# Kernel optimization log

Hardware: AMD Instinct MI355X
Metric: run time of the kernel (lower is better)

The kernel has to match this reference:

```python
import jax, jax.numpy as jnp
import numpy as np

EPS = 1e-5

def layer_norm(x, w, b):
    mu = x.mean(-1, keepdims=True)
    var = x.var(-1, keepdims=True)
    return (x - mu) / jnp.sqrt(var + EPS) * w + b

def moe_ffn(y, gW, W1, b1, W2, b2, topk):
    # y: [B,N,d]; W1: [E,d,f]; W2: [E,f,d].  Dense-equivalent of the
    # torch gather/compute/scatter-add dispatch: every expert runs on every
    # token, combined with top-k gate weights (zero for unselected experts).
    gate = jax.nn.softmax(y @ gW, axis=-1)                       # [B,N,E]
    w, sel = jax.lax.top_k(gate, topk)                           # [B,N,k]
    onehot = jax.nn.one_hot(sel, gW.shape[-1], dtype=y.dtype)    # [B,N,k,E]
    comb = jnp.einsum('bnk,bnke->bne', w, onehot)                # combine weights
    hmid = jax.nn.gelu(jnp.einsum('bnd,edf->bnef', y, W1) + b1, approximate=False)
    eo = jnp.einsum('bnef,efd->bned', hmid, W2) + b2             # [B,N,E,d]
    out = jnp.einsum('bne,bned->bnd', comb, eo)
    mask = onehot.sum(2)                                         # [B,N,E] 0/1
    cnt = mask.sum((0, 1))                                       # tokens per expert
    emb = jnp.einsum('bne,bnd->ed', mask, y) / jnp.maximum(cnt, 1.0)[:, None]
    return out, gate, emb

def setup_inputs():
    B, S, N = 8, 512, 1024
    d, H, E, f, L, topk = 512, 8, 8, 8, 2, 2   # d_ff == n_heads (repo quirk)
    key = jax.random.key(0)
    ks = iter(jax.random.split(key, 40))
    g = lambda shape, s=0.02: jax.random.normal(next(ks), shape, jnp.float32) * s
    return dict(
        x=jax.random.normal(next(ks), (B, S, N), jnp.float32),
        revin_w=jnp.ones((N,), jnp.float32) + g((N,), 0.01),
        revin_b=g((N,), 0.01),
        emb_W=g((S, d)), emb_b=g((d,)),
        Wq=g((L, d, d)), bq=g((L, d)),
        Wk=g((L, d, d)), bk=g((L, d)),
        Wv=g((L, d, d)), bv=g((L, d)),
        Wo=g((L, d, d)), bo=g((L, d)),
        ln1_w=jnp.ones((L, d), jnp.float32), ln1_b=jnp.zeros((L, d), jnp.float32),
        ln2_w=jnp.ones((L, d), jnp.float32), ln2_b=jnp.zeros((L, d), jnp.float32),
        gate_W=g((L, d, E)),
        eW1=g((L, E, d, f)), eb1=g((L, E, f)),
        eW2=g((L, E, f, d)), eb2=g((L, E, d)),
        enc_norm_w=jnp.ones((d,), jnp.float32), enc_norm_b=jnp.zeros((d,), jnp.float32),
        head_gate_W=g((d, E)),
        head_W=g((E, d, d)), head_b=g((E, d)),
        topk=topk, n_heads=H,
    )

def reference(x, revin_w, revin_b, emb_W, emb_b, Wq, bq, Wk, bk, Wv, bv, Wo, bo,
              ln1_w, ln1_b, ln2_w, ln2_b, gate_W, eW1, eb1, eW2, eb2,
              enc_norm_w, enc_norm_b, head_gate_W, head_W, head_b, topk, n_heads):
    B, S, N = x.shape
    d = emb_W.shape[1]
    H = n_heads
    dh = d // H
    L = Wq.shape[0]
    # RevIN normalize over time per variable (dropout layers are eval/identity)
    xv = jnp.swapaxes(x, 1, 2)                                   # [B,N,S]
    mean = xv.mean(-1, keepdims=True)
    std = jnp.sqrt(xv.var(-1, keepdims=True) + EPS)
    xn = (xv - mean) / std * revin_w[None, :, None] + revin_b[None, :, None]
    # DataEmbedding_inverted: Linear over the time axis -> variable tokens
    h = xn @ emb_W + emb_b                                       # [B,N,d]
    for l in range(L):
        q = (h @ Wq[l] + bq[l]).reshape(B, N, H, dh)
        k = (h @ Wk[l] + bk[l]).reshape(B, N, H, dh)
        v = (h @ Wv[l] + bv[l]).reshape(B, N, H, dh)
        attn = jax.nn.softmax(jnp.einsum('bnhe,bmhe->bhnm', q, k) / jnp.sqrt(jnp.float32(dh)), axis=-1)
        o = jnp.einsum('bhnm,bmhe->bnhe', attn, v).reshape(B, N, d) @ Wo[l] + bo[l]
        h = layer_norm(h + o, ln1_w[l], ln1_b[l])
        ffn, _gate, _emb = moe_ffn(h, gate_W[l], eW1[l], eb1[l], eW2[l], eb2[l], topk)
        h = layer_norm(h + ffn, ln2_w[l], ln2_b[l])
    h = layer_norm(h, enc_norm_w, enc_norm_b)
    # MoE projection head: experts are Linear(d, d)
    gate = jax.nn.softmax(h @ head_gate_W, axis=-1)
    w, sel = jax.lax.top_k(gate, topk)
    onehot = jax.nn.one_hot(sel, head_gate_W.shape[-1], dtype=h.dtype)
    comb = jnp.einsum('bnk,bnke->bne', w, onehot)
    eo = jnp.einsum('bnd,edf->bnef', h, head_W) + head_b         # [B,N,E,d]
    out = jnp.einsum('bne,bned->bnd', comb, eo)                  # [B,N,d]
    # RevIN denorm applied on [B, d_model, N]
    o2 = jnp.swapaxes(out, 1, 2)
    o2 = (o2 - revin_b[None, None, :]) / (revin_w[None, None, :] + 1e-10)
    o2 = o2 * jnp.swapaxes(std, 1, 2) + jnp.swapaxes(mean, 1, 2)
    return jnp.swapaxes(o2, 1, 2)                                # [B, n_vars, d_model]
```

## Files before the change

kernel.cpp:

```cpp
#include <hip/hip_runtime.h>
#include <math.h>

#define BATCH 8
#define SEQ 512
#define NVAR 1024
#define DM 512
#define NH 8
#define DH 64
#define NE 8
#define NF 8
#define NL 2
#define NTOK (BATCH*NVAR)
#define LN_EPS 1e-5f
#define LSC 2048.0f
#define ILSC (1.0f/2048.0f)

typedef __attribute__((ext_vector_type(8))) _Float16 f16x8;
typedef __attribute__((ext_vector_type(4))) float f32x4;
#define MFMA16 __builtin_amdgcn_mfma_f32_16x16x32_f16

__device__ __forceinline__ void fsplit(float v, _Float16& hi, _Float16& lo) {
    hi = (_Float16)v;
    lo = (_Float16)((v - (float)hi) * LSC);
}
__device__ __forceinline__ float frec(_Float16 hi, _Float16 lo) {
    return (float)hi + (float)lo * ILSC;
}

__device__ __forceinline__ void gload_lds16(const _Float16* g, _Float16* l) {
    __builtin_amdgcn_global_load_lds(
        (const __attribute__((address_space(1))) void*)g,
        (__attribute__((address_space(3))) void*)l, 16, 0, 0);
}

#define DPPROR(v, C) __int_as_float(__builtin_amdgcn_update_dpp(0, __float_as_int(v), (C), 0xF, 0xF, true))
__device__ __forceinline__ float rowmax16(float v) {
    v = fmaxf(v, DPPROR(v, 0x121));
    v = fmaxf(v, DPPROR(v, 0x122));
    v = fmaxf(v, DPPROR(v, 0x124));
    v = fmaxf(v, DPPROR(v, 0x128));
    return v;
}
__device__ __forceinline__ float rowsum16(float v) {
    v += DPPROR(v, 0x121);
    v += DPPROR(v, 0x122);
    v += DPPROR(v, 0x124);
    v += DPPROR(v, 0x128);
    return v;
}

__global__ __launch_bounds__(256) void revin_stats_kernel(
        const float* __restrict__ x, float* __restrict__ mean, float* __restrict__ stdd) {
    int blk = blockIdx.x;
    int b = blk >> 4;
    int n0 = (blk & 15) << 6;
    int t = threadIdx.x;
    int ni = t & 63, sg = t >> 6;
    float s = 0.f, ss = 0.f;
    for (int sidx = sg; sidx < SEQ; sidx += 4) {
        float v = x[((size_t)b*SEQ + sidx)*NVAR + n0 + ni];
        s += v; ss += v*v;
    }
    __shared__ float rs[4][64], rq[4][64];
    rs[sg][ni] = s; rq[sg][ni] = ss;
    __syncthreads();
    if (t < 64) {
        float su = rs[0][t] + rs[1][t] + rs[2][t] + rs[3][t];
        float sq = rq[0][t] + rq[1][t] + rq[2][t] + rq[3][t];
        float m  = su / (float)SEQ;
        float var = sq / (float)SEQ - m*m;
        int n = n0 + t;
        mean[b*NVAR + n] = m;
        stdd[b*NVAR + n] = sqrtf(var + LN_EPS);
    }
}

__global__ __launch_bounds__(256) void revin_norm_kernel(
        const float* __restrict__ x, const float* __restrict__ mean, const float* __restrict__ stdd,
        const float* __restrict__ rw, const float* __restrict__ rb,
        _Float16* __restrict__ xnhi, _Float16* __restrict__ xnlo) {
    __shared__ float tile[32][33];
    int n0 = blockIdx.x << 5, s0 = blockIdx.y << 5, b = blockIdx.z;
    int t = threadIdx.x;
    int j = t & 31, i0 = t >> 5;
    for (int ii = i0; ii < 32; ii += 8)
        tile[ii][j] = x[((size_t)b*SEQ + s0 + ii)*NVAR + n0 + j];
    __syncthreads();
    int si = t & 31, j0 = t >> 5;
    for (int nj = j0; nj < 32; nj += 8) {
        int n = n0 + nj;
        float m = mean[b*NVAR + n], sd = stdd[b*NVAR + n];
        float v = (tile[si][nj] - m) / sd * rw[n] + rb[n];
        _Float16 h_, l_; fsplit(v, h_, l_);
        size_t idx = ((size_t)b*NVAR + n)*SEQ + s0 + si;
        xnhi[idx] = h_; xnlo[idx] = l_;
    }
}

struct WSrcs { const float* p[9]; };
__global__ __launch_bounds__(256) void transpose_w_kernel(
        WSrcs srcs, _Float16* __restrict__ whi, _Float16* __restrict__ wlo) {
    const float* W = srcs.p[blockIdx.z];
    _Float16* oh = whi + (size_t)blockIdx.z * DM * DM;
    _Float16* ol = wlo + (size_t)blockIdx.z * DM * DM;
    __shared__ float tile[64][65];
    int k0 = blockIdx.x << 6, n0 = blockIdx.y << 6;
    int t = threadIdx.x;
    for (int idx = t; idx < 4096; idx += 256) {
        int k = idx >> 6, n = idx & 63;
        tile[k][n] = W[(size_t)(k0 + k)*DM + n0 + n];
    }
    __syncthreads();
    for (int idx = t; idx < 4096; idx += 256) {
        int n = idx >> 6, k = idx & 63;
        _Float16 h_, l_; fsplit(tile[k][n], h_, l_);
        size_t o = (size_t)(n0 + n)*DM + k0 + k;
        oh[o] = h_; ol[o] = l_;
    }
}

__global__ __launch_bounds__(256) void gemm_f16x2_kernel(
        const _Float16* __restrict__ Ahg, const _Float16* __restrict__ Alg,
        const _Float16* __restrict__ Whg, const _Float16* __restrict__ Wlg,
        const float* __restrict__ bias, float* __restrict__ C,
        _Float16* __restrict__ Chi, _Float16* __restrict__ Clo,
        int M, int K, int N) {
    __shared__ _Float16 sAh[128][32], sAl[128][32];
    __shared__ _Float16 sBh[64][32],  sBl[64][32];
    int id = blockIdx.x + (blockIdx.y << 3);
    int rm = ((id & 7) << 6) | (id >> 3);
    int bm = (rm >> 3) << 7, bn = (rm & 7) << 6;
    int t = threadIdx.x;
    int w = t >> 6, lane = t & 63, m16 = lane & 15, quad = lane >> 4;
    int wv = __builtin_amdgcn_readfirstlane(w);
    int lrow = lane >> 2, lcol = (lane & 3) << 3;
    f32x4 a1[2][4] = {}, a2[2][4] = {};
    for (int k0 = 0; k0 < K; k0 += 32) {
#pragma unroll
        for (int c = 0; c < 2; ++c) {
            size_t ga = (size_t)(bm + wv*32 + c*16 + lrow)*K + k0 + lcol;
            gload_lds16(&Ahg[ga], &sAh[wv*32 + c*16][0]);
            gload_lds16(&Alg[ga], &sAl[wv*32 + c*16][0]);
        }
        size_t gb = (size_t)(bn + wv*16 + lrow)*K + k0 + lcol;
        gload_lds16(&Whg[gb], &sBh[wv*16][0]);
        gload_lds16(&Wlg[gb], &sBl[wv*16][0]);
        __syncthreads();
        f16x8 bh_[4], bl_[4];
#pragma unroll
        for (int nt = 0; nt < 4; ++nt) {
            bh_[nt] = *(const f16x8*)&sBh[nt*16 + m16][quad*8];
            bl_[nt] = *(const f16x8*)&sBl[nt*16 + m16][quad*8];
        }
#pragma unroll
        for (int h2 = 0; h2 < 2; ++h2) {
            f16x8 ah = *(const f16x8*)&sAh[w*32 + h2*16 + m16][quad*8];
            f16x8 al = *(const f16x8*)&sAl[w*32 + h2*16 + m16][quad*8];
#pragma unroll
            for (int nt = 0; nt < 4; ++nt) {
                a1[h2][nt] = MFMA16(ah, bh_[nt], a1[h2][nt], 0, 0, 0);
                a2[h2][nt] = MFMA16(ah, bl_[nt], a2[h2][nt], 0, 0, 0);
                a2[h2][nt] = MFMA16(al, bh_[nt], a2[h2][nt], 0, 0, 0);
            }
        }
        __syncthreads();
    }
#pragma unroll
    for (int h2 = 0; h2 < 2; ++h2)
#pragma unroll
        for (int nt = 0; nt < 4; ++nt) {
            int col = bn + nt*16 + m16;
            float bv = bias[col];
#pragma unroll
            for (int r = 0; r < 4; ++r) {
                size_t row = bm + w*32 + h2*16 + quad*4 + r;
                float v = a1[h2][nt][r] + a2[h2][nt][r]*ILSC + bv;
                if (C) C[row*N + col] = v;
                if (Chi) {
                    _Float16 h_, l_; fsplit(v, h_, l_);
                    Chi[row*N + col] = h_; Clo[row*N + col] = l_;
                }
            }
        }
}

__global__ __launch_bounds__(256) void gemm_f16x2_vt_kernel(
        const _Float16* __restrict__ Ahg, const _Float16* __restrict__ Alg,
        const _Float16* __restrict__ Whg, const _Float16* __restrict__ Wlg,
        const float* __restrict__ bias,
        _Float16* __restrict__ vthi, _Float16* __restrict__ vtlo) {
    __shared__ _Float16 sAh[128][32], sAl[128][32];
    __shared__ _Float16 sBh[64][32],  sBl[64][32];
    __shared__ float Ct[128][65];
    int id = blockIdx.x + (blockIdx.y << 3);
    int rm = ((id & 7) << 6) | (id >> 3);
    int bm = (rm >> 3) << 7, bn = (rm & 7) << 6;
    int t = threadIdx.x;
    int w = t >> 6, lane = t & 63, m16 = lane & 15, quad = lane >> 4;
    int wv = __builtin_amdgcn_readfirstlane(w);
    int lrow = lane >> 2, lcol = (lane & 3) << 3;
    f32x4 a1[2][4] = {}, a2[2][4] = {};
    for (int k0 = 0; k0 < DM; k0 += 32) {
#pragma unroll
        for (int c = 0; c < 2; ++c) {
            size_t ga = (size_t)(bm + wv*32 + c*16 + lrow)*DM + k0 + lcol;
            gload_lds16(&Ahg[ga], &sAh[wv*32 + c*16][0]);
            gload_lds16(&Alg[ga], &sAl[wv*32 + c*16][0]);
        }
        size_t gb = (size_t)(bn + wv*16 + lrow)*DM + k0 + lcol;
        gload_lds16(&Whg[gb], &sBh[wv*16][0]);
        gload_lds16(&Wlg[gb], &sBl[wv*16][0]);
        __syncthreads();
        f16x8 bh_[4], bl_[4];
#pragma unroll
        for (int nt = 0; nt < 4; ++nt) {
            bh_[nt] = *(const f16x8*)&sBh[nt*16 + m16][quad*8];
            bl_[nt] = *(const f16x8*)&sBl[nt*16 + m16][quad*8];
        }
#pragma unroll
        for (int h2 = 0; h2 < 2; ++h2) {
            f16x8 ah = *(const f16x8*)&sAh[w*32 + h2*16 + m16][quad*8];
            f16x8 al = *(const f16x8*)&sAl[w*32 + h2*16 + m16][quad*8];
#pragma unroll
            for (int nt = 0; nt < 4; ++nt) {
                a1[h2][nt] = MFMA16(ah, bh_[nt], a1[h2][nt], 0, 0, 0);
                a2[h2][nt] = MFMA16(ah, bl_[nt], a2[h2][nt], 0, 0, 0);
                a2[h2][nt] = MFMA16(al, bh_[nt], a2[h2][nt], 0, 0, 0);
            }
        }
        __syncthreads();
    }
#pragma unroll
    for (int h2 = 0; h2 < 2; ++h2)
#pragma unroll
        for (int nt = 0; nt < 4; ++nt) {
            float bv = bias[bn + nt*16 + m16];
#pragma unroll
            for (int r = 0; r < 4; ++r)
                Ct[w*32 + h2*16 + quad*4 + r][nt*16 + m16] = a1[h2][nt][r] + a2[h2][nt][r]*ILSC + bv;
        }
    __syncthreads();
    int b = bm >> 10, tokn0 = bm & 1023, hh = bn >> 6;
    int dh = t >> 2, tg = (t & 3) << 4;
    size_t rowb = ((size_t)(b*8 + hh)*64 + dh)*NVAR + tokn0;
    for (int hb = 0; hb < 2; ++hb) {
        int tl0 = hb*64 + tg;
        unsigned short hbuf[16], lbuf[16];
#pragma unroll
        for (int i = 0; i < 16; ++i) {
            _Float16 h_, l_; fsplit(Ct[tl0 + i][dh], h_, l_);
            hbuf[i] = __builtin_bit_cast(unsigned short, h_);
            lbuf[i] = __builtin_bit_cast(unsigned short, l_);
        }
        uint4 uh0, uh1, ul0, ul1;
        uh0.x = hbuf[0]|(hbuf[1]<<16);  uh0.y = hbuf[2]|(hbuf[3]<<16);
        uh0.z = hbuf[4]|(hbuf[5]<<16);  uh0.w = hbuf[6]|(hbuf[7]<<16);
        uh1.x = hbuf[8]|(hbuf[9]<<16);  uh1.y = hbuf[10]|(hbuf[11]<<16);
        uh1.z = hbuf[12]|(hbuf[13]<<16);uh1.w = hbuf[14]|(hbuf[15]<<16);
        ul0.x = lbuf[0]|(lbuf[1]<<16);  ul0.y = lbuf[2]|(lbuf[3]<<16);
        ul0.z = lbuf[4]|(lbuf[5]<<16);  ul0.w = lbuf[6]|(lbuf[7]<<16);
        ul1.x = lbuf[8]|(lbuf[9]<<16);  ul1.y = lbuf[10]|(lbuf[11]<<16);
        ul1.z = lbuf[12]|(lbuf[13]<<16);ul1.w = lbuf[14]|(lbuf[15]<<16);
        *(uint4*)&vthi[rowb + tl0]     = uh0;
        *(uint4*)&vthi[rowb + tl0 + 8] = uh1;
        *(uint4*)&vtlo[rowb + tl0]     = ul0;
        *(uint4*)&vtlo[rowb + tl0 + 8] = ul1;
    }
}

__global__ __launch_bounds__(256, 4) void attn_f16x2_kernel(
        const _Float16* __restrict__ qh, const _Float16* __restrict__ ql,
        const _Float16* __restrict__ kh, const _Float16* __restrict__ kl,
        const _Float16* __restrict__ vth, const _Float16* __restrict__ vtl,
        _Float16* __restrict__ oh, _Float16* __restrict__ ol) {
    __shared__ _Float16 Kh[64][72], Kl[64][72];
    __shared__ _Float16 Vh[64][72], Vl[64][72];
    int blk = blockIdx.x;
    blk = ((blk & 7) << 7) | (blk >> 3);
    int qt = blk & 15, bh = blk >> 4;
    int b = bh >> 3, hh = bh & 7;
    int q0 = qt << 6;
    int t = threadIdx.x;
    int w = t >> 6, lane = t & 63;
    int m16 = lane & 15, quad = lane >> 4;
    size_t bbase = (size_t)b * NVAR;
    size_t vbase = (size_t)bh * DH * NVAR;

    f16x8 qfh[2], qfl[2];
#pragma unroll
    for (int ks = 0; ks < 2; ++ks) {
        size_t gq = (bbase + q0 + w*16 + m16)*DM + hh*DH + ks*32 + quad*8;
        qfh[ks] = *(const f16x8*)&qh[gq] * (_Float16)0.125f;
        qfl[ks] = *(const f16x8*)&ql[gq] * (_Float16)0.125f;
    }

    float mrow[4] = {-1e30f,-1e30f,-1e30f,-1e30f};
    float lrow[4] = {0.f,0.f,0.f,0.f};
    f32x4 o1[4] = {}, o2[4] = {};

    for (int n0 = 0; n0 < NVAR; n0 += 64) {
        for (int idx = t; idx < 512; idx += 256) {
            int r = idx >> 3, cg = (idx & 7) << 3;
            size_t gk = (bbase + n0 + r)*DM + hh*DH + cg;
            size_t gv = vbase + (size_t)r*NVAR + n0 + cg;
            *(uint4*)&Kh[r][cg] = *(const uint4*)&kh[gk];
            *(uint4*)&Kl[r][cg] = *(const uint4*)&kl[gk];
            *(uint4*)&Vh[r][cg] = *(const uint4*)&vth[gv];
            *(uint4*)&Vl[r][cg] = *(const uint4*)&vtl[gv];
        }
        __syncthreads();

        f32x4 s1[4] = {}, s2[4] = {};
#pragma unroll
        for (int ks = 0; ks < 2; ++ks) {
#pragma unroll
            for (int nt = 0; nt < 4; ++nt) {
                f16x8 bh_ = *(const f16x8*)&Kh[nt*16 + m16][ks*32 + quad*8];
                f16x8 bl_ = *(const f16x8*)&Kl[nt*16 + m16][ks*32 + quad*8];
                s1[nt] = MFMA16(qfh[ks], bh_, s1[nt], 0, 0, 0);
                s2[nt] = MFMA16(qfh[ks], bl_, s2[nt], 0, 0, 0);
                s2[nt] = MFMA16(qfl[ks], bh_, s2[nt], 0, 0, 0);
            }
        }
        __syncthreads();

        float pbuf[4][4];
        float mx[4];
#pragma unroll
        for (int r = 0; r < 4; ++r) {
            float sv0 = fmaf(s2[0][r], ILSC, s1[0][r]);
            float sv1 = fmaf(s2[1][r], ILSC, s1[1][r]);
            float sv2 = fmaf(s2[2][r], ILSC, s1[2][r]);
            float sv3 = fmaf(s2[3][r], ILSC, s1[3][r]);
            pbuf[0][r] = sv0; pbuf[1][r] = sv1; pbuf[2][r] = sv2; pbuf[3][r] = sv3;
            mx[r] = rowmax16(fmaxf(fmaxf(sv0, sv1), fmaxf(sv2, sv3)));
        }
        bool grow = (mx[0] > mrow[0]) | (mx[1] > mrow[1]) |
                    (mx[2] > mrow[2]) | (mx[3] > mrow[3]);
        if (__any(grow)) {
#pragma unroll
            for (int r = 0; r < 4; ++r) {
                float mnew = fmaxf(mrow[r], mx[r]);
                float alpha = __expf(mrow[r] - mnew);
                mrow[r] = mnew;
                lrow[r] *= alpha;
#pragma unroll
                for (int nt = 0; nt < 4; ++nt) { o1[nt][r] *= alpha; o2[nt][r] *= alpha; }
            }
        }
#pragma unroll
        for (int r = 0; r < 4; ++r) {
            float p0 = __expf(pbuf[0][r] - mrow[r]);
            float p1 = __expf(pbuf[1][r] - mrow[r]);
            float p2 = __expf(pbuf[2][r] - mrow[r]);
            float p3 = __expf(pbuf[3][r] - mrow[r]);
            lrow[r] += rowsum16(p0 + p1 + p2 + p3);
            pbuf[0][r] = p0; pbuf[1][r] = p1; pbuf[2][r] = p2; pbuf[3][r] = p3;
        }
#pragma unroll
        for (int nt = 0; nt < 4; ++nt)
#pragma unroll
            for (int r = 0; r < 4; ++r) {
                _Float16 h_, l_; fsplit(pbuf[nt][r], h_, l_);
                Kh[w*16 + quad*4 + r][nt*16 + m16] = h_;
                Kl[w*16 + quad*4 + r][nt*16 + m16] = l_;
            }

#pragma unroll
        for (int ks = 0; ks < 2; ++ks) {
            f16x8 ph = *(const f16x8*)&Kh[w*16 + m16][ks*32 + quad*8];
            f16x8 pl = *(const f16x8*)&Kl[w*16 + m16][ks*32 + quad*8];
#pragma unroll
            for (int nt = 0; nt < 4; ++nt) {
                f16x8 vh_ = *(const f16x8*)&Vh[nt*16 + m16][ks*32 + quad*8];
                f16x8 vl_ = *(const f16x8*)&Vl[nt*16 + m16][ks*32 + quad*8];
                o1[nt] = MFMA16(ph, vh_, o1[nt], 0, 0, 0);
                o2[nt] = MFMA16(ph, vl_, o2[nt], 0, 0, 0);
                o2[nt] = MFMA16(pl, vh_, o2[nt], 0, 0, 0);
            }
        }
        __syncthreads();
    }
#pragma unroll
    for (int r = 0; r < 4; ++r) {
        float inv = 1.0f / lrow[r];
        size_t rowp = (bbase + q0 + w*16 + quad*4 + r)*DM + hh*DH;
#pragma unroll
        for (int nt = 0; nt < 4; ++nt) {
            float ov = fmaf(o2[nt][r], ILSC, o1[nt][r]) * inv;
            _Float16 h_, l_; fsplit(ov, h_, l_);
            oh[rowp + nt*16 + m16] = h_;
            ol[rowp + nt*16 + m16] = l_;
        }
    }
}

__global__ __launch_bounds__(256) void ln_kernel(
        _Float16* __restrict__ hhi, _Float16* __restrict__ hlo,
        const float* __restrict__ res,
        const float* __restrict__ w, const float* __restrict__ b) {
    int rowi = blockIdx.x, t = threadIdx.x;
    size_t base = (size_t)rowi * DM;
    int c = t << 1;
    unsigned int uh = *(const unsigned int*)&hhi[base + c];
    unsigned int ul = *(const unsigned int*)&hlo[base + c];
    _Float16 h0 = __builtin_bit_cast(_Float16, (unsigned short)(uh & 0xFFFF));
    _Float16 h1 = __builtin_bit_cast(_Float16, (unsigned short)(uh >> 16));
    _Float16 l0 = __builtin_bit_cast(_Float16, (unsigned short)(ul & 0xFFFF));
    _Float16 l1 = __builtin_bit_cast(_Float16, (unsigned short)(ul >> 16));
    float v0 = frec(h0, l0);
    float v1 = frec(h1, l1);
    if (res) { float2 rv = *(const float2*)&res[base + c]; v0 += rv.x; v1 += rv.y; }
    float s = v0 + v1, q = v0*v0 + v1*v1;
#pragma unroll
    for (int off = 1; off < 64; off <<= 1) {
        s += __shfl_xor(s, off);
        q += __shfl_xor(q, off);
    }
    __shared__ float sred[4], qred[4];
    int wid = t >> 6, lane = t & 63;
    if (lane == 0) { sred[wid] = s; qred[wid] = q; }
    __syncthreads();
    s = sred[0] + sred[1] + sred[2] + sred[3];
    q = qred[0] + qred[1] + qred[2] + qred[3];
    float m = s / (float)DM;
    float var = q / (float)DM - m*m;
    float inv = 1.0f / sqrtf(var + LN_EPS);
    float2 wv = *(const float2*)&w[c];
    float2 bv = *(const float2*)&b[c];
    float y0 = (v0 - m)*inv * wv.x + bv.x;
    float y1 = (v1 - m)*inv * wv.y + bv.y;
    _Float16 h0o, l0o, h1o, l1o;
    fsplit(y0, h0o, l0o); fsplit(y1, h1o, l1o);
    *(unsigned int*)&hhi[base + c] =
        (unsigned int)__builtin_bit_cast(unsigned short, h0o) |
        ((unsigned int)__builtin_bit_cast(unsigned short, h1o) << 16);
    *(unsigned int*)&hlo[base + c] =
        (unsigned int)__builtin_bit_cast(unsigned short, l0o) |
        ((unsigned int)__builtin_bit_cast(unsigned short, l1o) << 16);
}

__device__ __forceinline__ float gelu_exact(float xv) {
    return 0.5f * xv * (1.0f + erff(xv * 0.70710678118654752f));
}

__global__ __launch_bounds__(256) void moe_kernel(
        const _Float16* __restrict__ hhi, const _Float16* __restrict__ hlo,
        float* __restrict__ out,
        const float* __restrict__ gW, const float* __restrict__ W1, const float* __restrict__ b1,
        const float* __restrict__ W2, const float* __restrict__ b2) {
    int tok = blockIdx.x, t = threadIdx.x;
    __shared__ float hs[DM];
    __shared__ float red[32][8];
    __shared__ float glog[8];
    __shared__ float hmid[8];
    __shared__ float wsel[2];
    __shared__ int   esel[2];
    size_t base = (size_t)tok * DM;
    hs[t] = frec(hhi[base + t], hlo[base + t]);
    hs[t + 256] = frec(hhi[base + t + 256], hlo[base + t + 256]);
    __syncthreads();
    int e = t & 7, i0 = t >> 3;
    {
        float a = 0.f;
        for (int i = i0; i < DM; i += 32) a += hs[i] * gW[i*NE + e];
        red[i0][e] = a;
    }
    __syncthreads();
    if (t < 8) { float sv = 0.f; for (int i = 0; i < 32; ++i) sv += red[i][t]; glog[t] = sv; }
    __syncthreads();
    if (t == 0) {
        float m0 = -1e30f, m1 = -1e30f; int s0i = 0, s1i = 0;
        for (int ei = 0; ei < 8; ++ei) {
            float vv = glog[ei];
            if (vv > m0) { m1 = m0; s1i = s0i; m0 = vv; s0i = ei; }
            else if (vv > m1) { m1 = vv; s1i = ei; }
        }
        float Z = 0.f;
        for (int ei = 0; ei < 8; ++ei) Z += expf(glog[ei] - m0);
        wsel[0] = 1.0f / Z;
        wsel[1] = expf(m1 - m0) / Z;
        esel[0] = s0i; esel[1] = s1i;
    }
    __syncthreads();
    float o0 = 0.f, o1 = 0.f;
    for (int ks = 0; ks < 2; ++ks) {
        int ee = esel[ks]; float wk = wsel[ks];
        int f = t & 7;
        float a = 0.f;
        for (int i = i0; i < DM; i += 32) a += hs[i] * W1[((size_t)ee*DM + i)*NF + f];
        red[i0][f] = a;
        __syncthreads();
        if (t < 8) {
            float sv = b1[ee*NF + t];
            for (int i = 0; i < 32; ++i) sv += red[i][t];
            hmid[t] = gelu_exact(sv);
        }
        __syncthreads();
        float s0v = b2[ee*DM + t], s1v = b2[ee*DM + t + 256];
#pragma unroll
        for (int i = 0; i < NF; ++i) {
            float hm = hmid[i];
            const float* wp = W2 + ((size_t)ee*NF + i)*DM;
            s0v += hm * wp[t]; s1v += hm * wp[t + 256];
        }
        o0 += wk * s0v; o1 += wk * s1v;
        __syncthreads();
    }
    out[base + t] = o0; out[base + t + 256] = o1;
}

__global__ __launch_bounds__(64) void head_init_kernel(int* __restrict__ cnt) {
    if (threadIdx.x < NE) cnt[threadIdx.x] = 0;
}

__global__ __launch_bounds__(256) void head_gate_kernel(
        const _Float16* __restrict__ hhi, const _Float16* __restrict__ hlo,
        const float* __restrict__ gW,
        int* __restrict__ sel, float2* __restrict__ wpair) {
    int tok = blockIdx.x, t = threadIdx.x;
    __shared__ float hs[DM];
    __shared__ float red[32][8];
    __shared__ float glog[8];
    size_t base = (size_t)tok * DM;
    hs[t] = frec(hhi[base + t], hlo[base + t]);
    hs[t + 256] = frec(hhi[base + t + 256], hlo[base + t + 256]);
    __syncthreads();
    int e = t & 7, i0 = t >> 3;
    float a = 0.f;
    for (int i = i0; i < DM; i += 32) a += hs[i] * gW[i*NE + e];
    red[i0][e] = a;
    __syncthreads();
    if (t < 8) { float sv = 0.f; for (int i = 0; i < 32; ++i) sv += red[i][t]; glog[t] = sv; }
    __syncthreads();
    if (t == 0) {
        float m0 = -1e30f, m1 = -1e30f; int s0i = 0, s1i = 0;
        for (int ei = 0; ei < 8; ++ei) {
            float vv = glog[ei];
            if (vv > m0) { m1 = m0; s1i = s0i; m0 = vv; s0i = ei; }
            else if (vv > m1) { m1 = vv; s1i = ei; }
        }
        float Z = 0.f;
        for (int ei = 0; ei < 8; ++ei) Z += __expf(glog[ei] - m0);
        float2 wv;
        wv.x = 1.0f / Z;
        wv.y = __expf(m1 - m0) / Z;
        sel[tok] = s0i | (s1i << 3);
        wpair[tok] = wv;
    }
}

__global__ __launch_bounds__(64) void head_bucket_kernel(
        const int* __restrict__ sel, const float2* __restrict__ wpair,
        int* __restrict__ cnt, int* __restrict__ idxlist, float* __restrict__ wlist,
        int* __restrict__ pos0, int* __restrict__ pos1) {
    int lane = threadIdx.x;
    int tok = blockIdx.x*64 + lane;
    int s = sel[tok];
    int s0 = s & 7, s1 = (s >> 3) & 7;
    float2 wv = wpair[tok];
    unsigned long long lmask = (lane == 63) ? 0x7FFFFFFFFFFFFFFFull
                                            : ((1ull << lane) - 1ull);
#pragma unroll
    for (int e = 0; e < NE; ++e) {
        unsigned long long m0 = __ballot(s0 == e);
        unsigned long long m1 = __ballot(s1 == e);
        int tot = __popcll(m0) + __popcll(m1);
        int basep = 0;
        if (lane == 0 && tot > 0) basep = atomicAdd(&cnt[e], tot);
        basep = __shfl(basep, 0);
        if (s0 == e) {
            int p = basep + __popcll(m0 & lmask);
            idxlist[e*NTOK + p] = tok; wlist[e*NTOK + p] = wv.x;
            pos0[tok] = (e << 16) | p;
        }
        if (s1 == e) {
            int p = basep + __popcll(m0) + __popcll(m1 & lmask);
            idxlist[e*NTOK + p] = tok; wlist[e*NTOK + p] = wv.y;
            pos1[tok] = (e << 16) | p;
        }
    }
}

__global__ __launch_bounds__(64) void head_prefix_kernel(int* __restrict__ cnt) {
    if (threadIdx.x == 0) {
        int run = 0, trun = 0;
        for (int e = 0; e < NE; ++e) {
            cnt[8 + e]  = run;  run  += cnt[e];
            cnt[16 + e] = trun; trun += (cnt[e] + 63) >> 6;
        }
        cnt[24] = trun;
    }
}

__global__ __launch_bounds__(256) void head_gemm_f16x2_kernel(
        const _Float16* __restrict__ hhi, const _Float16* __restrict__ hlo,
        const _Float16* __restrict__ hwhi, const _Float16* __restrict__ hwlo,
        const float* __restrict__ Hb,
        const int* __restrict__ cnt, const int* __restrict__ idxlist,
        const float* __restrict__ wlist, float* __restrict__ slotf) {
    int item = blockIdx.x;
    int total = cnt[24];
    if (item >= 2*total) return;
    int bn   = (item & 1) << 8;
    int tile = item >> 1;
    int e = 0;
#pragma unroll
    for (int ei = 1; ei < NE; ++ei) if (tile >= cnt[16 + ei]) e = ei;
    int m0 = (tile - cnt[16 + e]) << 6;
    int cnt_e = cnt[e];
    int rv = cnt_e - m0; if (rv > 64) rv = 64;
    int pref_e = cnt[8 + e];
    int t = threadIdx.x;
    int w = t >> 6, lane = t & 63, m16 = lane & 15, quad = lane >> 4;

    __shared__ _Float16 sAh[64][40], sAl[64][40];
    __shared__ _Float16 sBh[256][40], sBl[256][40];
    __shared__ int   idxs[64];
    __shared__ float ws[64];
    if (t < 64) {
        if (t < rv) { idxs[t] = idxlist[e*NTOK + m0 + t]; ws[t] = wlist[e*NTOK + m0 + t]; }
        else        { idxs[t] = idxlist[e*NTOK + m0];     ws[t] = 0.f; }
    }
    __syncthreads();

    const _Float16* Wh = hwhi + (size_t)e*DM*DM;
    const _Float16* Wl = hwlo + (size_t)e*DM*DM;
    int ra = t >> 2, ca = (t & 3) << 3;
    f32x4 a1[4][4] = {}, a2[4][4] = {};
    for (int k0 = 0; k0 < DM; k0 += 32) {
        size_t ga = (size_t)idxs[ra]*DM + k0 + ca;
        *(uint4*)&sAh[ra][ca] = *(const uint4*)&hhi[ga];
        *(uint4*)&sAl[ra][ca] = *(const uint4*)&hlo[ga];
#pragma unroll
        for (int p = 0; p < 4; ++p) {
            int rb = p*64 + ra;
            size_t gb = (size_t)(bn + rb)*DM + k0 + ca;
            *(uint4*)&sBh[rb][ca] = *(const uint4*)&Wh[gb];
            *(uint4*)&sBl[rb][ca] = *(const uint4*)&Wl[gb];
        }
        __syncthreads();
        f16x8 ah[4], al[4];
#pragma unroll
        for (int mt = 0; mt < 4; ++mt) {
            ah[mt] = *(const f16x8*)&sAh[mt*16 + m16][quad*8];
            al[mt] = *(const f16x8*)&sAl[mt*16 + m16][quad*8];
        }
#pragma unroll
        for (int nt = 0; nt < 4; ++nt) {
            f16x8 bh_ = *(const f16x8*)&sBh[w*64 + nt*16 + m16][quad*8];
            f16x8 bl_ = *(const f16x8*)&sBl[w*64 + nt*16 + m16][quad*8];
#pragma unroll
            for (int mt = 0; mt < 4; ++mt) {
                a1[mt][nt] = MFMA16(ah[mt], bh_, a1[mt][nt], 0, 0, 0);
                a2[mt][nt] = MFMA16(ah[mt], bl_, a2[mt][nt], 0, 0, 0);
                a2[mt][nt] = MFMA16(al[mt], bh_, a2[mt][nt], 0, 0, 0);
            }
        }
        __syncthreads();
    }
#pragma unroll
    for (int mt = 0; mt < 4; ++mt)
#pragma unroll
        for (int r = 0; r < 4; ++r) {
            int rloc = mt*16 + quad*4 + r;
            if (rloc < rv) {
                float wk = ws[rloc];
                size_t srow = (size_t)(pref_e + m0 + rloc)*DM;
#pragma unroll
                for (int nt = 0; nt < 4; ++nt) {
                    int gcol = bn + w*64 + nt*16 + m16;
                    float v = a1[mt][nt][r] + a2[mt][nt][r]*ILSC + Hb[e*DM + gcol];
                    slotf[srow + gcol] = wk * v;
                }
            }
        }
}

__global__ __launch_bounds__(256) void head_combine_kernel(
        const float* __restrict__ slotf,
        const int* __restrict__ pos0, const int* __restrict__ pos1,
        const int* __restrict__ cnt,
        const float* __restrict__ rw, const float* __restrict__ rb,
        const float* __restrict__ mean, const float* __restrict__ stdd,
        float* __restrict__ out) {
    int tok = blockIdx.x, t = threadIdx.x;
    int n = tok & (NVAR - 1);
    int e0enc = pos0[tok], e1enc = pos1[tok];
    size_t s0 = (size_t)(cnt[8 + (e0enc >> 16)] + (e0enc & 0xFFFF)) * DM;
    size_t s1 = (size_t)(cnt[8 + (e1enc >> 16)] + (e1enc & 0xFFFF)) * DM;
    size_t base = (size_t)tok * DM;
    float mn = mean[tok], sd = stdd[tok];
    float rwv = rw[n] + 1e-10f, rbv = rb[n];
    float o0 = slotf[s0 + t] + slotf[s1 + t];
    float o1 = slotf[s0 + t + 256] + slotf[s1 + t + 256];
    out[base + t]       = (o0 - rbv) / rwv * sd + mn;
    out[base + t + 256] = (o1 - rbv) / rwv * sd + mn;
}

extern "C" void kernel_launch(void* const* d_in, const int* in_sizes, int n_in,
                              void* d_out, int out_size, void* d_ws, size_t ws_size,
                              hipStream_t stream) {
    const float* x       = (const float*)d_in[0];
    const float* revin_w = (const float*)d_in[1];
    const float* revin_b = (const float*)d_in[2];
    const float* emb_W   = (const float*)d_in[3];
    const float* emb_b   = (const float*)d_in[4];
    const float* Wq      = (const float*)d_in[5];
    const float* bq      = (const float*)d_in[6];
    const float* Wk      = (const float*)d_in[7];
    const float* bk      = (const float*)d_in[8];
    const float* Wv      = (const float*)d_in[9];
    const float* bv      = (const float*)d_in[10];
    const float* Wo      = (const float*)d_in[11];
    const float* bo      = (const float*)d_in[12];
    const float* ln1_w   = (const float*)d_in[13];
    const float* ln1_b   = (const float*)d_in[14];
    const float* ln2_w   = (const float*)d_in[15];
    const float* ln2_b   = (const float*)d_in[16];
    const float* gate_W  = (const float*)d_in[17];
    const float* eW1     = (const float*)d_in[18];
    const float* eb1     = (const float*)d_in[19];
    const float* eW2     = (const float*)d_in[20];
    const float* eb2     = (const float*)d_in[21];
    const float* enc_w   = (const float*)d_in[22];
    const float* enc_b   = (const float*)d_in[23];
    const float* hgW     = (const float*)d_in[24];
    const float* hW      = (const float*)d_in[25];
    const float* hb      = (const float*)d_in[26];
    float* out = (float*)d_out;

    const size_t TOKD = (size_t)NTOK * DM;
    float* ws   = (float*)d_ws;
    float* mean = ws;
    float* stdd = ws + 8192;
    _Float16* hhi  = (_Float16*)(ws + 16384);
    _Float16* hlo  = hhi + TOKD;
    _Float16* qhi  = hlo + TOKD;
    _Float16* qlo  = qhi + TOKD;
    _Float16* khi  = qlo + TOKD;
    _Float16* klo  = khi + TOKD;
    _Float16* vthi = klo + TOKD;
    _Float16* vtlo = vthi + TOKD;
    _Float16* whi  = vtlo + TOKD;
    _Float16* wlo  = whi + (size_t)9*DM*DM;
    int*   cnt     = (int*)(wlo + (size_t)9*DM*DM);
    int*   idxlist = cnt + 32;
    float* wlist   = (float*)(idxlist + NE*NTOK);
    int*   sel     = (int*)(wlist + NE*NTOK);
    float2* wpair  = (float2*)(sel + NTOK);
    int*   pos0    = (int*)(wpair + NTOK);
    int*   pos1    = pos0 + NTOK;
    float* proj    = (float*)khi;
    float* slotf   = (float*)qhi;

    dim3 blk(256);
    dim3 ggemm(DM/64, NTOK/128);

    revin_stats_kernel<<<dim3(BATCH*16), blk, 0, stream>>>(x, mean, stdd);
    revin_norm_kernel<<<dim3(NVAR/32, SEQ/32, BATCH), blk, 0, stream>>>(
        x, mean, stdd, revin_w, revin_b, qhi, qlo);

    WSrcs srcs;
    srcs.p[0] = emb_W;
    for (int l = 0; l < NL; ++l) {
        srcs.p[1 + l*4 + 0] = Wq + (size_t)l*DM*DM;
        srcs.p[1 + l*4 + 1] = Wk + (size_t)l*DM*DM;
        srcs.p[1 + l*4 + 2] = Wv + (size_t)l*DM*DM;
        srcs.p[1 + l*4 + 3] = Wo + (size_t)l*DM*DM;
    }
    transpose_w_kernel<<<dim3(8, 8, 9), blk, 0, stream>>>(srcs, whi, wlo);

    gemm_f16x2_kernel<<<ggemm, blk, 0, stream>>>(
        qhi, qlo, whi, wlo, emb_b, nullptr, hhi, hlo, NTOK, SEQ, DM);

    for (int l = 0; l < NL; ++l) {
        size_t oq = (size_t)(1 + l*4 + 0)*DM*DM;
        size_t ok = (size_t)(1 + l*4 + 1)*DM*DM;
        size_t ov = (size_t)(1 + l*4 + 2)*DM*DM;
        size_t oo = (size_t)(1 + l*4 + 3)*DM*DM;
        gemm_f16x2_kernel<<<ggemm, blk, 0, stream>>>(
            hhi, hlo, whi + oq, wlo + oq, bq + l*DM, nullptr, qhi, qlo, NTOK, DM, DM);
        gemm_f16x2_kernel<<<ggemm, blk, 0, stream>>>(
            hhi, hlo, whi + ok, wlo + ok, bk + l*DM, nullptr, khi, klo, NTOK, DM, DM);
        gemm_f16x2_vt_kernel<<<ggemm, blk, 0, stream>>>(
            hhi, hlo, whi + ov, wlo + ov, bv + l*DM, vthi, vtlo);
        attn_f16x2_kernel<<<dim3(64*16), blk, 0, stream>>>(
            qhi, qlo, khi, klo, vthi, vtlo, qhi, qlo);
        gemm_f16x2_kernel<<<ggemm, blk, 0, stream>>>(
            qhi, qlo, whi + oo, wlo + oo, bo + l*DM, proj, nullptr, nullptr, NTOK, DM, DM);
        ln_kernel<<<dim3(NTOK), blk, 0, stream>>>(hhi, hlo, proj, ln1_w + l*DM, ln1_b + l*DM);
        moe_kernel<<<dim3(NTOK), blk, 0, stream>>>(
            hhi, hlo, proj, gate_W + (size_t)l*DM*NE,
            eW1 + (size_t)l*NE*DM*NF, eb1 + (size_t)l*NE*NF,
            eW2 + (size_t)l*NE*NF*DM, eb2 + (size_t)l*NE*DM);
        ln_kernel<<<dim3(NTOK), blk, 0, stream>>>(hhi, hlo, proj, ln2_w + l*DM, ln2_b + l*DM);
    }

    ln_kernel<<<dim3(NTOK), blk, 0, stream>>>(hhi, hlo, nullptr, enc_w, enc_b);

    WSrcs hsrcs;
    for (int e = 0; e < NE; ++e) hsrcs.p[e] = hW + (size_t)e*DM*DM;
    hsrcs.p[8] = hW;
    transpose_w_kernel<<<dim3(8, 8, 8), blk, 0, stream>>>(hsrcs, vthi, vtlo);

    head_init_kernel<<<dim3(1), dim3(64), 0, stream>>>(cnt);
    head_gate_kernel<<<dim3(NTOK), blk, 0, stream>>>(hhi, hlo, hgW, sel, wpair);
    head_bucket_kernel<<<dim3(NTOK/64), dim3(64), 0, stream>>>(
        sel, wpair, cnt, idxlist, wlist, pos0, pos1);
    head_prefix_kernel<<<dim3(1), dim3(64), 0, stream>>>(cnt);
    head_gemm_f16x2_kernel<<<dim3(576), blk, 0, stream>>>(
        hhi, hlo, vthi, vtlo, hb, cnt, idxlist, wlist, slotf);
    head_combine_kernel<<<dim3(NTOK), blk, 0, stream>>>(
        slotf, pos0, pos1, cnt, revin_w, revin_b, mean, stdd, out);
}
```

Before: 854.8 us.

## Double-buffer LDS tiles in split-f16 GEMM kernels to overlap loads with MFMA

Both split-precision GEMM kernels now keep two LDS stages: the next K-slice is loaded into the alternate buffer while MFMAs run on the current one. This cuts the two barriers per iteration down to one. The goal is to hide global-to-LDS latency behind compute. In exchange, LDS use per block in the plain GEMM grows to 48KB, which may lower occupancy. The transpose kernel reuses the same buffer for its output staging tile.

```diff
diff --git a/kernel.cpp b/kernel.cpp
--- a/kernel.cpp
+++ b/kernel.cpp
@@ -125,8 +125,7 @@
         const float* __restrict__ bias, float* __restrict__ C,
         _Float16* __restrict__ Chi, _Float16* __restrict__ Clo,
         int M, int K, int N) {
-    __shared__ _Float16 sAh[128][32], sAl[128][32];
-    __shared__ _Float16 sBh[64][32],  sBl[64][32];
+    __shared__ _Float16 smem[24576];
     int id = blockIdx.x + (blockIdx.y << 3);
     int rm = ((id & 7) << 6) | (id >> 3);
     int bm = (rm >> 3) << 7, bn = (rm & 7) << 6;
@@ -135,27 +134,38 @@
     int wv = __builtin_amdgcn_readfirstlane(w);
     int lrow = lane >> 2, lcol = (lane & 3) << 3;
     f32x4 a1[2][4] = {}, a2[2][4] = {};
-    for (int k0 = 0; k0 < K; k0 += 32) {
-#pragma unroll
-        for (int c = 0; c < 2; ++c) {
-            size_t ga = (size_t)(bm + wv*32 + c*16 + lrow)*K + k0 + lcol;
-            gload_lds16(&Ahg[ga], &sAh[wv*32 + c*16][0]);
-            gload_lds16(&Alg[ga], &sAl[wv*32 + c*16][0]);
-        }
-        size_t gb = (size_t)(bn + wv*16 + lrow)*K + k0 + lcol;
-        gload_lds16(&Whg[gb], &sBh[wv*16][0]);
-        gload_lds16(&Wlg[gb], &sBl[wv*16][0]);
-        __syncthreads();
+
+    #define G_STAGE(c, kk) do {                                              \
+        _Pragma("unroll")                                                    \
+        for (int ch = 0; ch < 2; ++ch) {                                     \
+            size_t ga = (size_t)(bm + wv*32 + ch*16 + lrow)*K + (kk) + lcol; \
+            gload_lds16(&Ahg[ga], &smem[(c)*4096 + (wv*32 + ch*16)*32]);     \
+            gload_lds16(&Alg[ga], &smem[8192 + (c)*4096 + (wv*32 + ch*16)*32]); \
+        }                                                                    \
+        size_t gb = (size_t)(bn + wv*16 + lrow)*K + (kk) + lcol;             \
+        gload_lds16(&Whg[gb], &smem[16384 + (c)*2048 + (wv*16)*32]);         \
+        gload_lds16(&Wlg[gb], &smem[20480 + (c)*2048 + (wv*16)*32]);         \
+    } while (0)
+
+    G_STAGE(0, 0);
+    int cur = 0;
+    for (int k0 = 0; k0 < K; k0 += 32, cur ^= 1) {
+        __syncthreads();
+        if (k0 + 32 < K) G_STAGE(cur ^ 1, k0 + 32);
+        const _Float16* AH = &smem[cur*4096];
+        const _Float16* AL = &smem[8192 + cur*4096];
+        const _Float16* BH = &smem[16384 + cur*2048];
+        const _Float16* BL = &smem[20480 + cur*2048];
         f16x8 bh_[4], bl_[4];
 #pragma unroll
         for (int nt = 0; nt < 4; ++nt) {
-            bh_[nt] = *(const f16x8*)&sBh[nt*16 + m16][quad*8];
-            bl_[nt] = *(const f16x8*)&sBl[nt*16 + m16][quad*8];
+            bh_[nt] = *(const f16x8*)&BH[(nt*16 + m16)*32 + quad*8];
+            bl_[nt] = *(const f16x8*)&BL[(nt*16 + m16)*32 + quad*8];
         }
 #pragma unroll
         for (int h2 = 0; h2 < 2; ++h2) {
-            f16x8 ah = *(const f16x8*)&sAh[w*32 + h2*16 + m16][quad*8];
-            f16x8 al = *(const f16x8*)&sAl[w*32 + h2*16 + m16][quad*8];
+            f16x8 ah = *(const f16x8*)&AH[(w*32 + h2*16 + m16)*32 + quad*8];
+            f16x8 al = *(const f16x8*)&AL[(w*32 + h2*16 + m16)*32 + quad*8];
 #pragma unroll
             for (int nt = 0; nt < 4; ++nt) {
                 a1[h2][nt] = MFMA16(ah, bh_[nt], a1[h2][nt], 0, 0, 0);
@@ -163,8 +173,8 @@
                 a2[h2][nt] = MFMA16(al, bh_[nt], a2[h2][nt], 0, 0, 0);
             }
         }
-        __syncthreads();
-    }
+    }
+    #undef G_STAGE
 #pragma unroll
     for (int h2 = 0; h2 < 2; ++h2)
 #pragma unroll
@@ -189,9 +199,7 @@
         const _Float16* __restrict__ Whg, const _Float16* __restrict__ Wlg,
         const float* __restrict__ bias,
         _Float16* __restrict__ vthi, _Float16* __restrict__ vtlo) {
-    __shared__ _Float16 sAh[128][32], sAl[128][32];
-    __shared__ _Float16 sBh[64][32],  sBl[64][32];
-    __shared__ float Ct[128][65];
+    __shared__ _Float16 smem[24576];
     int id = blockIdx.x + (blockIdx.y << 3);
     int rm = ((id & 7) << 6) | (id >> 3);
     int bm = (rm >> 3) << 7, bn = (rm & 7) << 6;
@@ -200,27 +208,38 @@
     int wv = __builtin_amdgcn_readfirstlane(w);
     int lrow = lane >> 2, lcol = (lane & 3) << 3;
     f32x4 a1[2][4] = {}, a2[2][4] = {};
-    for (int k0 = 0; k0 < DM; k0 += 32) {
-#pragma unroll
-        for (int c = 0; c < 2; ++c) {
-            size_t ga = (size_t)(bm + wv*32 + c*16 + lrow)*DM + k0 + lcol;
-            gload_lds16(&Ahg[ga], &sAh[wv*32 + c*16][0]);
-            gload_lds16(&Alg[ga], &sAl[wv*32 + c*16][0]);
-        }
-        size_t gb = (size_t)(bn + wv*16 + lrow)*DM + k0 + lcol;
-        gload_lds16(&Whg[gb], &sBh[wv*16][0]);
-        gload_lds16(&Wlg[gb], &sBl[wv*16][0]);
-        __syncthreads();
+
+    #define G_STAGE(c, kk) do {                                              \
+        _Pragma("unroll")                                                    \
+        for (int ch = 0; ch < 2; ++ch) {                                     \
+            size_t ga = (size_t)(bm + wv*32 + ch*16 + lrow)*DM + (kk) + lcol;\
+            gload_lds16(&Ahg[ga], &smem[(c)*4096 + (wv*32 + ch*16)*32]);     \
+            gload_lds16(&Alg[ga], &smem[8192 + (c)*4096 + (wv*32 + ch*16)*32]); \
+        }                                                                    \
+        size_t gb = (size_t)(bn + wv*16 + lrow)*DM + (kk) + lcol;            \
+        gload_lds16(&Whg[gb], &smem[16384 + (c)*2048 + (wv*16)*32]);         \
+        gload_lds16(&Wlg[gb], &smem[20480 + (c)*2048 + (wv*16)*32]);         \
+    } while (0)
+
+    G_STAGE(0, 0);
+    int cur = 0;
+    for (int k0 = 0; k0 < DM; k0 += 32, cur ^= 1) {
+        __syncthreads();
+        if (k0 + 32 < DM) G_STAGE(cur ^ 1, k0 + 32);
+        const _Float16* AH = &smem[cur*4096];
+        const _Float16* AL = &smem[8192 + cur*4096];
+        const _Float16* BH = &smem[16384 + cur*2048];
+        const _Float16* BL = &smem[20480 + cur*2048];
         f16x8 bh_[4], bl_[4];
 #pragma unroll
         for (int nt = 0; nt < 4; ++nt) {
-            bh_[nt] = *(const f16x8*)&sBh[nt*16 + m16][quad*8];
-            bl_[nt] = *(const f16x8*)&sBl[nt*16 + m16][quad*8];
+            bh_[nt] = *(const f16x8*)&BH[(nt*16 + m16)*32 + quad*8];
+            bl_[nt] = *(const f16x8*)&BL[(nt*16 + m16)*32 + quad*8];
         }
 #pragma unroll
         for (int h2 = 0; h2 < 2; ++h2) {
-            f16x8 ah = *(const f16x8*)&sAh[w*32 + h2*16 + m16][quad*8];
-            f16x8 al = *(const f16x8*)&sAl[w*32 + h2*16 + m16][quad*8];
+            f16x8 ah = *(const f16x8*)&AH[(w*32 + h2*16 + m16)*32 + quad*8];
+            f16x8 al = *(const f16x8*)&AL[(w*32 + h2*16 + m16)*32 + quad*8];
 #pragma unroll
             for (int nt = 0; nt < 4; ++nt) {
                 a1[h2][nt] = MFMA16(ah, bh_[nt], a1[h2][nt], 0, 0, 0);
@@ -228,8 +247,10 @@
                 a2[h2][nt] = MFMA16(al, bh_[nt], a2[h2][nt], 0, 0, 0);
             }
         }
-        __syncthreads();
-    }
+    }
+    #undef G_STAGE
+    __syncthreads();
+    float (*Ct)[65] = (float (*)[65])smem;
 #pragma unroll
     for (int h2 = 0; h2 < 2; ++h2)
 #pragma unroll
```

Result: faster. 826.0 us (-3.4%).
